# Performance work log

Measured on AMD Instinct MI355X. Metric: run time of the kernel, lower is better.

The kernel has to match this reference:

```python
import jax, jax.numpy as jnp
import numpy as np

N_NODES = 100000
N_EDGES = 1600000
IN_DIM = 256
HID = 128
ALPHA = 0.1
K_STEPS = 10


def setup_inputs() -> dict:
    key = jax.random.key(0)
    ks = jax.random.split(key, 10)
    x = jax.random.normal(ks[0], (N_NODES, IN_DIM), dtype=jnp.float32)
    edge_index = jax.random.randint(ks[1], (2, N_EDGES), 0, N_NODES, dtype=jnp.int64)
    s = 0.02
    W1 = jax.random.normal(ks[2], (HID, IN_DIM), dtype=jnp.float32) * s
    b1 = jnp.zeros((HID,), dtype=jnp.float32)
    W2 = jax.random.normal(ks[3], (HID, HID), dtype=jnp.float32) * s
    b2 = jnp.zeros((HID,), dtype=jnp.float32)
    W3 = jax.random.normal(ks[4], (HID, HID), dtype=jnp.float32) * s
    b3 = jnp.zeros((HID,), dtype=jnp.float32)
    Wo = jax.random.normal(ks[5], (1, HID), dtype=jnp.float32) * s
    bo = jnp.zeros((1,), dtype=jnp.float32)
    return {"x": x, "edge_index": edge_index, "W1": W1, "b1": b1,
            "W2": W2, "b2": b2, "W3": W3, "b3": b3, "Wo": Wo, "bo": bo}


def _gcn_norm(edge_index, num_nodes):
    # add self-loops, then symmetric normalization 1/sqrt(deg_i * deg_j)
    loop = jnp.arange(num_nodes, dtype=edge_index.dtype)
    src = jnp.concatenate([edge_index[0], loop])
    dst = jnp.concatenate([edge_index[1], loop])
    ones = jnp.ones(src.shape[0], dtype=jnp.float32)
    deg = jax.ops.segment_sum(ones, dst, num_segments=num_nodes)
    dinv = jnp.where(deg > 0, jax.lax.rsqrt(deg), 0.0)
    norm = dinv[src] * dinv[dst]
    return src, dst, norm


def reference(x, edge_index, W1, b1, W2, b2, W3, b3, Wo, bo):
    # MLP encoder (dropout=0 -> identity in eval)
    h = jax.nn.relu(x @ W1.T + b1)
    h = jax.nn.relu(h @ W2.T + b2)
    h = jax.nn.relu(h @ W3.T + b3)
    # APPNP propagation: h <- (1-alpha) * A_hat h + alpha * h0
    n = x.shape[0]
    src, dst, norm = _gcn_norm(edge_index, n)
    h0 = h
    for _ in range(K_STEPS):
        msg = norm[:, None] * h[src]            # [E+N, HID]
        agg = jax.ops.segment_sum(msg, dst, num_segments=n)
        h = (1.0 - ALPHA) * agg + ALPHA * h0
    out = h @ Wo.T + bo                          # [N, 1]
    return out.squeeze(-1)
```

## Files before the change

### kernel.cpp

```cpp
#include <hip/hip_runtime.h>

#define NN   100000
#define NE   1600000
#define IND  256
#define HIDD 128
#define BCAP 64
#define NPART 196
#define SCAP 10240
#define APITCH 40
#define HPITCH 136
#define NGE  1563

typedef __attribute__((ext_vector_type(8))) short short8v;
typedef __attribute__((ext_vector_type(4))) float f32x4;

__device__ inline unsigned packbf2(float x, float y) {
  unsigned xb = __float_as_uint(x);
  unsigned yb = __float_as_uint(y);
  xb += 0x7fffu + ((xb >> 16) & 1u);
  yb += 0x7fffu + ((yb >> 16) & 1u);
  return (xb >> 16) | (yb & 0xffff0000u);
}
__device__ inline unsigned short bf16r(float x) {
  unsigned b = __float_as_uint(x);
  b += 0x7fffu + ((b >> 16) & 1u);
  return (unsigned short)(b >> 16);
}

__global__ void wcvt_all(const float* __restrict__ W1, const float* __restrict__ W2,
                         const float* __restrict__ W3, unsigned* __restrict__ W1b,
                         unsigned* __restrict__ W2b, unsigned* __restrict__ W3b,
                         int* __restrict__ gcur) {
  int i = blockIdx.x * 256 + threadIdx.x;
  if (i < NPART) gcur[i] = 0;
  const float* src; unsigned* dst; int off;
  if (i < 16384)      { src = W1; dst = W1b; off = i; }
  else if (i < 24576) { src = W2; dst = W2b; off = i - 16384; }
  else                { src = W3; dst = W3b; off = i - 24576; }
  float2 v = ((const float2*)src)[off];
  dst[off] = packbf2(v.x, v.y);
}

__global__ __launch_bounds__(256) void enc_fillA(
    const float* __restrict__ x,
    const unsigned short* __restrict__ W1b, const float* __restrict__ b1,
    const unsigned short* __restrict__ W2b, const float* __restrict__ b2,
    const unsigned short* __restrict__ W3b, const float* __restrict__ b3,
    const float* __restrict__ Wo, float* __restrict__ z,
    const int* __restrict__ src, const int* __restrict__ dst,
    int* __restrict__ gcur, unsigned* __restrict__ sbuf)
{
  __shared__ unsigned short hbuf[64 * HPITCH];
  __shared__ float zsh[2][64];
  __shared__ int hist[NPART];
  __shared__ int lofs[NPART];
  const int tid = threadIdx.x;
  const int bid = blockIdx.x;
  const int r3v = bid % 3;

  if (r3v == 2) {
    int fi = bid / 3;
    const int base = fi * 2048;
    for (int i = tid; i < NPART; i += 256) hist[i] = 0;
    __syncthreads();
    int d[8], s[8];
#pragma unroll
    for (int i = 0; i < 8; ++i) {
      int e = base + i * 256 + tid;
      bool v = e < NE;
      d[i] = v ? dst[e] : -1;
      s[i] = v ? src[e] : 0;
      if (v) atomicAdd(&hist[d[i] >> 9], 1);
    }
    __syncthreads();
    for (int i = tid; i < NPART; i += 256)
      lofs[i] = hist[i] ? atomicAdd(&gcur[i], hist[i]) : 0;
    __syncthreads();
#pragma unroll
    for (int i = 0; i < 8; ++i) {
      if (d[i] >= 0) {
        int p = d[i] >> 9;
        int q = atomicAdd(&lofs[p], 1);
        if (q < SCAP)
          sbuf[(size_t)p * SCAP + q] = ((unsigned)(d[i] & 511) << 17) | (unsigned)s[i];
      }
    }
    return;
  }

  const int gb = (bid / 3) * 2 + r3v;
  if (gb >= NGE) return;
  unsigned short* lA = hbuf;
  const int lane = tid & 63, wid = tid >> 6;
  const int wr = wid >> 1, wc = wid & 1;
  const int bm = gb * 64;
  const int lr = lane & 15, lg = lane >> 4;

  f32x4 acc[2][4];
#pragma unroll
  for (int i = 0; i < 2; ++i)
#pragma unroll
    for (int j = 0; j < 4; ++j) acc[i][j] = (f32x4){0.f, 0.f, 0.f, 0.f};

  for (int k0 = 0; k0 < IND; k0 += 32) {
    {
      int rr = tid >> 2, g = tid & 3;
      int grow = bm + rr;
      float4 v0 = make_float4(0.f, 0.f, 0.f, 0.f), v1 = v0;
      if (grow < NN) {
        const float* ap = x + (size_t)grow * IND + k0 + g * 8;
        v0 = ((const float4*)ap)[0]; v1 = ((const float4*)ap)[1];
      }
      uint4 pk;
      pk.x = packbf2(v0.x, v0.y); pk.y = packbf2(v0.z, v0.w);
      pk.z = packbf2(v1.x, v1.y); pk.w = packbf2(v1.z, v1.w);
      *(uint4*)&lA[rr * APITCH + g * 8] = pk;
    }
    __syncthreads();
    {
      short8v a[2], b[4];
#pragma unroll
      for (int i = 0; i < 2; ++i)
        a[i] = *(const short8v*)&lA[(wr * 32 + i * 16 + lr) * APITCH + lg * 8];
#pragma unroll
      for (int j = 0; j < 4; ++j)
        b[j] = *(const short8v*)&W1b[(size_t)(wc * 64 + j * 16 + lr) * IND + k0 + lg * 8];
#pragma unroll
      for (int i = 0; i < 2; ++i)
#pragma unroll
        for (int j = 0; j < 4; ++j)
          acc[i][j] = __builtin_amdgcn_mfma_f32_16x16x32_bf16(a[i], b[j], acc[i][j], 0, 0, 0);
    }
    __syncthreads();
  }
#pragma unroll
  for (int i = 0; i < 2; ++i)
#pragma unroll
    for (int e = 0; e < 4; ++e) {
      int lrow = wr * 32 + i * 16 + lg * 4 + e;
#pragma unroll
      for (int j = 0; j < 4; ++j) {
        int cc = wc * 64 + j * 16 + lr;
        hbuf[lrow * HPITCH + cc] = bf16r(fmaxf(acc[i][j][e] + b1[cc], 0.f));
      }
    }
  __syncthreads();

#pragma unroll
  for (int i = 0; i < 2; ++i)
#pragma unroll
    for (int j = 0; j < 4; ++j) acc[i][j] = (f32x4){0.f, 0.f, 0.f, 0.f};
  for (int k0 = 0; k0 < HIDD; k0 += 32) {
    short8v a[2], b[4];
#pragma unroll
    for (int i = 0; i < 2; ++i)
      a[i] = *(const short8v*)&hbuf[(wr * 32 + i * 16 + lr) * HPITCH + k0 + lg * 8];
#pragma unroll
    for (int j = 0; j < 4; ++j)
      b[j] = *(const short8v*)&W2b[(size_t)(wc * 64 + j * 16 + lr) * HIDD + k0 + lg * 8];
#pragma unroll
    for (int i = 0; i < 2; ++i)
#pragma unroll
      for (int j = 0; j < 4; ++j)
        acc[i][j] = __builtin_amdgcn_mfma_f32_16x16x32_bf16(a[i], b[j], acc[i][j], 0, 0, 0);
  }
  __syncthreads();
#pragma unroll
  for (int i = 0; i < 2; ++i)
#pragma unroll
    for (int e = 0; e < 4; ++e) {
      int lrow = wr * 32 + i * 16 + lg * 4 + e;
#pragma unroll
      for (int j = 0; j < 4; ++j) {
        int cc = wc * 64 + j * 16 + lr;
        hbuf[lrow * HPITCH + cc] = bf16r(fmaxf(acc[i][j][e] + b2[cc], 0.f));
      }
    }
  __syncthreads();

#pragma unroll
  for (int i = 0; i < 2; ++i)
#pragma unroll
    for (int j = 0; j < 4; ++j) acc[i][j] = (f32x4){0.f, 0.f, 0.f, 0.f};
  for (int k0 = 0; k0 < HIDD; k0 += 32) {
    short8v a[2], b[4];
#pragma unroll
    for (int i = 0; i < 2; ++i)
      a[i] = *(const short8v*)&hbuf[(wr * 32 + i * 16 + lr) * HPITCH + k0 + lg * 8];
#pragma unroll
    for (int j = 0; j < 4; ++j)
      b[j] = *(const short8v*)&W3b[(size_t)(wc * 64 + j * 16 + lr) * HIDD + k0 + lg * 8];
#pragma unroll
    for (int i = 0; i < 2; ++i)
#pragma unroll
      for (int j = 0; j < 4; ++j)
        acc[i][j] = __builtin_amdgcn_mfma_f32_16x16x32_bf16(a[i], b[j], acc[i][j], 0, 0, 0);
  }
  float wv[4];
#pragma unroll
  for (int j = 0; j < 4; ++j) wv[j] = Wo[wc * 64 + j * 16 + lr];
  if (tid < 128) { zsh[tid >> 6][tid & 63] = 0.f; }
  __syncthreads();
#pragma unroll
  for (int i = 0; i < 2; ++i)
#pragma unroll
    for (int e = 0; e < 4; ++e) {
      float part = 0.f;
#pragma unroll
      for (int j = 0; j < 4; ++j) {
        int cc = wc * 64 + j * 16 + lr;
        part += fmaxf(acc[i][j][e] + b3[cc], 0.f) * wv[j];
      }
#pragma unroll
      for (int off = 8; off > 0; off >>= 1) part += __shfl_down(part, off, 16);
      if (lr == 0) zsh[wc][wr * 32 + i * 16 + lg * 4 + e] = part;
    }
  __syncthreads();
  if (tid < 64) {
    int row = bm + tid;
    if (row < NN) z[row] = zsh[0][tid] + zsh[1][tid];
  }
}

__global__ __launch_bounds__(256, 8) void fill_phaseB(
    const unsigned* __restrict__ sbuf, const int* __restrict__ gcur,
    const float* __restrict__ z, int* __restrict__ colbuk,
    int* __restrict__ deg, float* __restrict__ dinv, float* __restrict__ va)
{
  __shared__ int lcur[512];
  const int tid = threadIdx.x;
  const int b = blockIdx.x;
  for (int i = tid; i < 512; i += 256) lcur[i] = 0;
  __syncthreads();
  int cnt = min(gcur[b], SCAP);
  const unsigned* sp = sbuf + (size_t)b * SCAP;
  for (int i = tid; i < cnt; i += 256) {
    unsigned u = sp[i];
    int dloc = (int)(u >> 17);
    int s = (int)(u & 0x1FFFFu);
    int pos = atomicAdd(&lcur[dloc], 1);
    if (pos < BCAP) colbuk[(size_t)((b << 9) + dloc) * BCAP + pos] = s;
  }
  __syncthreads();
  for (int i = tid; i < 512; i += 256) {
    int node = (b << 9) + i;
    if (node < NN) {
      int dg = lcur[i];
      float di = rsqrtf((float)(dg + 1));
      deg[node] = dg;
      dinv[node] = di;
      va[node] = di * z[node];
    }
  }
}

template<int LAST>
__global__ __launch_bounds__(256, 8) void appnp_sstep(
    const float* __restrict__ vin, const float* __restrict__ z,
    const float* __restrict__ dinv, const int* __restrict__ deg,
    const int* __restrict__ colbuk, float* __restrict__ vout,
    const float* __restrict__ bo, float* __restrict__ out)
{
  int tid = threadIdx.x;
  int sl = tid & 15;
  int node = blockIdx.x * 16 + (tid >> 4);
  if (node >= NN) return;
  int m = min(deg[node], BCAP);
  float val = (sl == 0) ? vin[node] : 0.f;
  for (int j = sl; j < m; j += 16)
    val += vin[colbuk[(size_t)node * BCAP + j]];
#pragma unroll
  for (int off = 8; off > 0; off >>= 1) val += __shfl_down(val, off, 16);
  if (sl == 0) {
    float di = dinv[node];
    float s = 0.9f * di * val + 0.1f * z[node];
    if (LAST) out[node] = s + bo[0];
    else vout[node] = di * s;
  }
}

extern "C" void kernel_launch(void* const* d_in, const int* in_sizes, int n_in,
                              void* d_out, int out_size, void* d_ws, size_t ws_size,
                              hipStream_t stream) {
  const float* x   = (const float*)d_in[0];
  const int*   ei  = (const int*)d_in[1];
  const float* W1  = (const float*)d_in[2];
  const float* b1  = (const float*)d_in[3];
  const float* W2  = (const float*)d_in[4];
  const float* b2  = (const float*)d_in[5];
  const float* W3  = (const float*)d_in[6];
  const float* b3  = (const float*)d_in[7];
  const float* Wo  = (const float*)d_in[8];
  const float* bo  = (const float*)d_in[9];
  float* out = (float*)d_out;

  const int* srcv = ei;
  const int* dstv = ei + NE;

  int*      colbuk = (int*)d_ws;
  unsigned* sbuf   = (unsigned*)(colbuk + (size_t)NN * BCAP);
  int*      gcur   = (int*)(sbuf + (size_t)NPART * SCAP);
  int*      deg    = gcur + NPART;
  float*    dinv   = (float*)(deg + NN);
  float*    zbuf   = dinv + NN;
  float*    va     = zbuf + NN;
  float*    vb     = va + NN;
  unsigned* W1b    = (unsigned*)(vb + NN);
  unsigned* W2b    = W1b + 16384;
  unsigned* W3b    = W2b + 8192;

  wcvt_all<<<128, 256, 0, stream>>>(W1, W2, W3, W1b, W2b, W3b, gcur);

  enc_fillA<<<2346, 256, 0, stream>>>(x, (unsigned short*)W1b, b1,
                                      (unsigned short*)W2b, b2,
                                      (unsigned short*)W3b, b3, Wo, zbuf,
                                      srcv, dstv, gcur, sbuf);

  fill_phaseB<<<NPART, 256, 0, stream>>>(sbuf, gcur, zbuf, colbuk, deg, dinv, va);

  int ssb = (NN + 15) / 16;
  float* cur = va; float* nxt = vb;
  for (int k = 0; k < 9; ++k) {
    appnp_sstep<0><<<ssb, 256, 0, stream>>>(cur, zbuf, dinv, deg, colbuk,
                                            nxt, nullptr, nullptr);
    float* t = cur; cur = nxt; nxt = t;
  }
  appnp_sstep<1><<<ssb, 256, 0, stream>>>(cur, zbuf, dinv, deg, colbuk,
                                          nullptr, bo, out);
}
```

Before: 204.9 us.

## Double-buffer x tiles in the encoder GEMM and preload W2/W3 fragments

The first MLP layer now uses two LDS buffers. The next 32-column slice of x is loaded from global memory while MFMAs run on the current slice, which halves the barriers per k-step. The W2 and W3 GEMMs issue all weight-fragment loads up front into registers before the MFMA loop, so the global-load latency is exposed less. This raises register pressure (16 extra short8 vectors plus prefetch registers), which could reduce occupancy.

Result: no change. 203.0 us (-0.9%).

```diff
diff --git a/kernel.cpp b/kernel.cpp
--- a/kernel.cpp
+++ b/kernel.cpp
@@ -90,7 +90,8 @@
 
   const int gb = (bid / 3) * 2 + r3v;
   if (gb >= NGE) return;
-  unsigned short* lA = hbuf;
+  unsigned short* lb0 = hbuf;
+  unsigned short* lb1 = hbuf + 2560;
   const int lane = tid & 63, wid = tid >> 6;
   const int wr = wid >> 1, wc = wid & 1;
   const int bm = gb * 64;
@@ -102,36 +103,52 @@
 #pragma unroll
     for (int j = 0; j < 4; ++j) acc[i][j] = (f32x4){0.f, 0.f, 0.f, 0.f};
 
-  for (int k0 = 0; k0 < IND; k0 += 32) {
+  {
+    const int rr = tid >> 2, g = tid & 3;
+    const int grow = bm + rr;
+    const bool rowok = (grow < NN);
+    const float* xrow = x + (size_t)(rowok ? grow : 0) * IND + g * 8;
     {
-      int rr = tid >> 2, g = tid & 3;
-      int grow = bm + rr;
       float4 v0 = make_float4(0.f, 0.f, 0.f, 0.f), v1 = v0;
-      if (grow < NN) {
-        const float* ap = x + (size_t)grow * IND + k0 + g * 8;
-        v0 = ((const float4*)ap)[0]; v1 = ((const float4*)ap)[1];
-      }
+      if (rowok) { v0 = ((const float4*)xrow)[0]; v1 = ((const float4*)xrow)[1]; }
       uint4 pk;
       pk.x = packbf2(v0.x, v0.y); pk.y = packbf2(v0.z, v0.w);
       pk.z = packbf2(v1.x, v1.y); pk.w = packbf2(v1.z, v1.w);
-      *(uint4*)&lA[rr * APITCH + g * 8] = pk;
+      *(uint4*)&lb0[rr * APITCH + g * 8] = pk;
     }
     __syncthreads();
-    {
-      short8v a[2], b[4];
-#pragma unroll
-      for (int i = 0; i < 2; ++i)
-        a[i] = *(const short8v*)&lA[(wr * 32 + i * 16 + lr) * APITCH + lg * 8];
-#pragma unroll
-      for (int j = 0; j < 4; ++j)
-        b[j] = *(const short8v*)&W1b[(size_t)(wc * 64 + j * 16 + lr) * IND + k0 + lg * 8];
-#pragma unroll
-      for (int i = 0; i < 2; ++i)
+#pragma unroll
+    for (int k = 0; k < 8; ++k) {
+      float4 n0 = make_float4(0.f, 0.f, 0.f, 0.f), n1 = n0;
+      if (k < 7 && rowok) {
+        const float* np = xrow + (k + 1) * 32;
+        n0 = ((const float4*)np)[0];
+        n1 = ((const float4*)np)[1];
+      }
+      {
+        const unsigned short* lc = (k & 1) ? lb1 : lb0;
+        short8v a[2], b[4];
+#pragma unroll
+        for (int i = 0; i < 2; ++i)
+          a[i] = *(const short8v*)&lc[(wr * 32 + i * 16 + lr) * APITCH + lg * 8];
 #pragma unroll
         for (int j = 0; j < 4; ++j)
-          acc[i][j] = __builtin_amdgcn_mfma_f32_16x16x32_bf16(a[i], b[j], acc[i][j], 0, 0, 0);
-    }
-    __syncthreads();
+          b[j] = *(const short8v*)&W1b[(size_t)(wc * 64 + j * 16 + lr) * IND + k * 32 + lg * 8];
+#pragma unroll
+        for (int i = 0; i < 2; ++i)
+#pragma unroll
+          for (int j = 0; j < 4; ++j)
+            acc[i][j] = __builtin_amdgcn_mfma_f32_16x16x32_bf16(a[i], b[j], acc[i][j], 0, 0, 0);
+      }
+      if (k < 7) {
+        unsigned short* ln = ((k + 1) & 1) ? lb1 : lb0;
+        uint4 pk;
+        pk.x = packbf2(n0.x, n0.y); pk.y = packbf2(n0.z, n0.w);
+        pk.z = packbf2(n1.x, n1.y); pk.w = packbf2(n1.z, n1.w);
+        *(uint4*)&ln[rr * APITCH + g * 8] = pk;
+      }
+      __syncthreads();
+    }
   }
 #pragma unroll
   for (int i = 0; i < 2; ++i)
@@ -150,19 +167,25 @@
   for (int i = 0; i < 2; ++i)
 #pragma unroll
     for (int j = 0; j < 4; ++j) acc[i][j] = (f32x4){0.f, 0.f, 0.f, 0.f};
-  for (int k0 = 0; k0 < HIDD; k0 += 32) {
-    short8v a[2], b[4];
-#pragma unroll
-    for (int i = 0; i < 2; ++i)
-      a[i] = *(const short8v*)&hbuf[(wr * 32 + i * 16 + lr) * HPITCH + k0 + lg * 8];
-#pragma unroll
-    for (int j = 0; j < 4; ++j)
-      b[j] = *(const short8v*)&W2b[(size_t)(wc * 64 + j * 16 + lr) * HIDD + k0 + lg * 8];
-#pragma unroll
-    for (int i = 0; i < 2; ++i)
+  {
+    short8v ball[16];
+#pragma unroll
+    for (int kk = 0; kk < 4; ++kk)
 #pragma unroll
       for (int j = 0; j < 4; ++j)
-        acc[i][j] = __builtin_amdgcn_mfma_f32_16x16x32_bf16(a[i], b[j], acc[i][j], 0, 0, 0);
+        ball[kk * 4 + j] = *(const short8v*)&W2b[(size_t)(wc * 64 + j * 16 + lr) * HIDD + kk * 32 + lg * 8];
+#pragma unroll
+    for (int kk = 0; kk < 4; ++kk) {
+      short8v a[2];
+#pragma unroll
+      for (int i = 0; i < 2; ++i)
+        a[i] = *(const short8v*)&hbuf[(wr * 32 + i * 16 + lr) * HPITCH + kk * 32 + lg * 8];
+#pragma unroll
+      for (int i = 0; i < 2; ++i)
+#pragma unroll
+        for (int j = 0; j < 4; ++j)
+          acc[i][j] = __builtin_amdgcn_mfma_f32_16x16x32_bf16(a[i], ball[kk * 4 + j], acc[i][j], 0, 0, 0);
+    }
   }
   __syncthreads();
 #pragma unroll
@@ -182,19 +205,25 @@
   for (int i = 0; i < 2; ++i)
 #pragma unroll
     for (int j = 0; j < 4; ++j) acc[i][j] = (f32x4){0.f, 0.f, 0.f, 0.f};
-  for (int k0 = 0; k0 < HIDD; k0 += 32) {
-    short8v a[2], b[4];
-#pragma unroll
-    for (int i = 0; i < 2; ++i)
-      a[i] = *(const short8v*)&hbuf[(wr * 32 + i * 16 + lr) * HPITCH + k0 + lg * 8];
-#pragma unroll
-    for (int j = 0; j < 4; ++j)
-      b[j] = *(const short8v*)&W3b[(size_t)(wc * 64 + j * 16 + lr) * HIDD + k0 + lg * 8];
-#pragma unroll
-    for (int i = 0; i < 2; ++i)
+  {
+    short8v ball[16];
+#pragma unroll
+    for (int kk = 0; kk < 4; ++kk)
 #pragma unroll
       for (int j = 0; j < 4; ++j)
-        acc[i][j] = __builtin_amdgcn_mfma_f32_16x16x32_bf16(a[i], b[j], acc[i][j], 0, 0, 0);
+        ball[kk * 4 + j] = *(const short8v*)&W3b[(size_t)(wc * 64 + j * 16 + lr) * HIDD + kk * 32 + lg * 8];
+#pragma unroll
+    for (int kk = 0; kk < 4; ++kk) {
+      short8v a[2];
+#pragma unroll
+      for (int i = 0; i < 2; ++i)
+        a[i] = *(const short8v*)&hbuf[(wr * 32 + i * 16 + lr) * HPITCH + kk * 32 + lg * 8];
+#pragma unroll
+      for (int i = 0; i < 2; ++i)
+#pragma unroll
+        for (int j = 0; j < 4; ++j)
+          acc[i][j] = __builtin_amdgcn_mfma_f32_16x16x32_bf16(a[i], ball[kk * 4 + j], acc[i][j], 0, 0, 0);
+    }
   }
   float wv[4];
 #pragma unroll
```
